# Optimization experiments

Hardware: AMD Instinct MI355X
Metric: run time of the kernel (lower is better)

## Reference

```python
import jax, jax.numpy as jnp
import numpy as np

NUM_LAYERS = 4


def setup_inputs() -> dict:
    key = jax.random.key(0)
    k1, k2, k3, k4 = jax.random.split(key, 4)
    num_users, num_items, D, E = 100000, 50000, 64, 2000000
    N = num_users + num_items
    emb_users = jax.random.normal(k1, (num_users, D), dtype=jnp.float32)
    emb_items = jax.random.normal(k2, (num_items, D), dtype=jnp.float32)
    src = jax.random.randint(k3, (E,), 0, N, dtype=jnp.int64)
    dst = jax.random.randint(k4, (E,), 0, N, dtype=jnp.int64)
    edge_index = jnp.stack([src, dst], axis=0)
    return {"emb_users": emb_users, "emb_items": emb_items, "edge_index": edge_index}


def _lightgcn(emb_users, emb_items, edge_index):
    num_users = emb_users.shape[0]
    num_items = emb_items.shape[0]
    N = num_users + num_items
    src, dst = edge_index[0], edge_index[1]

    # gcn_norm without self-loops (PyG LGConv default): deg over destination nodes
    ones = jnp.ones(src.shape[0], dtype=emb_users.dtype)
    deg = jax.ops.segment_sum(ones, dst, num_segments=N)
    deg_inv_sqrt = jnp.where(deg > 0, jax.lax.rsqrt(jnp.maximum(deg, 1.0)), 0.0)
    norm = deg_inv_sqrt[src] * deg_inv_sqrt[dst]  # [E]

    emb = jnp.concatenate([emb_users, emb_items], axis=0)  # [N, D]
    acc = emb
    for _ in range(NUM_LAYERS):
        msg = norm[:, None] * emb[src]  # [E, D]
        emb = jax.ops.segment_sum(msg, dst, num_segments=N)
        acc = acc + emb

    # original: 1/(L+1) * mean(stack, dim=1) == sum / (L+1)^2
    emb_final = acc / float((NUM_LAYERS + 1) ** 2)
    return emb_final[:num_users], emb_final[num_users:]


def reference(emb_users, emb_items, edge_index):
    return _lightgcn(emb_users, emb_items, edge_index)
```

## Files before the change

### kernel.cpp

```cpp
#include <hip/hip_runtime.h>
#include <hip/hip_bf16.h>

#define D 64
#define NUM_LAYERS 4
#define TILE 4096
#define BKMAX 320


__device__ __forceinline__ float bf_lo(unsigned u) { return __uint_as_float(u << 16); }
__device__ __forceinline__ float bf_hi(unsigned u) { return __uint_as_float(u & 0xffff0000u); }
__device__ __forceinline__ unsigned bf_pack(float x, float y) {
    __hip_bfloat16 bx = __float2bfloat16(x);
    __hip_bfloat16 by = __float2bfloat16(y);
    return (unsigned)(*reinterpret_cast<unsigned short*>(&bx))
         | ((unsigned)(*reinterpret_cast<unsigned short*>(&by)) << 16);
}


__global__ void bhist_kernel(const int* __restrict__ dst, int* __restrict__ bcnt, int E, int nbk) {
    __shared__ int h[BKMAX];
    for (int i = threadIdx.x; i < nbk; i += blockDim.x) h[i] = 0;
    __syncthreads();
    int stride = gridDim.x * blockDim.x;
    int gid = blockIdx.x * blockDim.x + threadIdx.x;
    int E4 = (((size_t)dst & 15) == 0) ? (E >> 2) : 0;
    const int4* dst4 = (const int4*)dst;
    for (int i = gid; i < E4; i += stride) {
        int4 d = dst4[i];
        atomicAdd(&h[d.x >> 9], 1);
        atomicAdd(&h[d.y >> 9], 1);
        atomicAdd(&h[d.z >> 9], 1);
        atomicAdd(&h[d.w >> 9], 1);
    }
    for (int e = (E4 << 2) + gid; e < E; e += stride)
        atomicAdd(&h[dst[e] >> 9], 1);
    __syncthreads();
    for (int i = threadIdx.x; i < nbk; i += blockDim.x)
        if (h[i] > 0) atomicAdd(&bcnt[i], h[i]);
}

__global__ __launch_bounds__(512) void bscan_kernel(const int* __restrict__ bcnt,
                                                    int* __restrict__ bstart,
                                                    int* __restrict__ gcur, int nbk, int E) {
    __shared__ int sm[512];
    int t = threadIdx.x;
    int v = (t < nbk) ? bcnt[t] : 0;
    sm[t] = v;
    __syncthreads();
    for (int ofs = 1; ofs < 512; ofs <<= 1) {
        int x = (t >= ofs) ? sm[t - ofs] : 0;
        __syncthreads();
        sm[t] += x;
        __syncthreads();
    }
    int excl = sm[t] - v;
    if (t < nbk) { bstart[t] = excl; gcur[t] = excl; }
    if (t == 0) bstart[nbk] = E;
}


__global__ __launch_bounds__(512) void placeA_kernel(const int* __restrict__ src,
                                                     const int* __restrict__ dst,
                                                     int* __restrict__ gcur,
                                                     int* __restrict__ mid,
                                                     int E, int nbk) {
    __shared__ int hist[BKMAX];
    __shared__ int toff[BKMAX];
    __shared__ int gbase[BKMAX];
    __shared__ int sc[512];
    __shared__ int els[TILE];
    __shared__ unsigned short bkt[TILE];
    int t = threadIdx.x;
    int tile0 = blockIdx.x * TILE;
    int tcnt = min(TILE, E - tile0);
    for (int i = t; i < nbk; i += 512) hist[i] = 0;
    __syncthreads();

    bool al = (((size_t)src & 15) == 0) && (((size_t)dst & 15) == 0);

    int p_[8];
    int b_[8];
    int r_[8];
#pragma unroll
    for (int i4 = 0; i4 < 2; ++i4) {
        int e0 = tile0 + i4 * 2048 + t * 4;
        int4 s4, d4;
        if (al && (e0 + 3 < E)) {
            s4 = *(const int4*)(src + e0);
            d4 = *(const int4*)(dst + e0);
        } else {
            s4 = make_int4(0, 0, 0, 0); d4 = make_int4(0, 0, 0, 0);
            if (e0     < E) { s4.x = src[e0];     d4.x = dst[e0]; }
            if (e0 + 1 < E) { s4.y = src[e0 + 1]; d4.y = dst[e0 + 1]; }
            if (e0 + 2 < E) { s4.z = src[e0 + 2]; d4.z = dst[e0 + 2]; }
            if (e0 + 3 < E) { s4.w = src[e0 + 3]; d4.w = dst[e0 + 3]; }
        }
        int ss[4] = { s4.x, s4.y, s4.z, s4.w };
        int dd[4] = { d4.x, d4.y, d4.z, d4.w };
#pragma unroll
        for (int k = 0; k < 4; ++k) {
            int i = i4 * 4 + k;
            int e = e0 + k;
            b_[i] = -1;
            if (e < E) {
                p_[i] = ss[k] | ((dd[k] & 511) << 18);
                b_[i] = dd[k] >> 9;
                r_[i] = atomicAdd(&hist[b_[i]], 1);
            }
        }
    }
    __syncthreads();
    int v = (t < nbk) ? hist[t] : 0;
    sc[t] = v;
    __syncthreads();
    for (int ofs = 1; ofs < 512; ofs <<= 1) {
        int x = (t >= ofs) ? sc[t - ofs] : 0;
        __syncthreads();
        sc[t] += x;
        __syncthreads();
    }
    if (t < nbk) toff[t] = sc[t] - v;
    __syncthreads();
#pragma unroll
    for (int i = 0; i < 8; ++i) {
        if (b_[i] >= 0) {
            int pos = toff[b_[i]] + r_[i];
            els[pos] = p_[i];
            bkt[pos] = (unsigned short)b_[i];
        }
    }
    for (int b = t; b < nbk; b += 512) {
        int h = hist[b];
        gbase[b] = (h > 0) ? atomicAdd(&gcur[b], h) : 0;
    }
    __syncthreads();
    for (int i = t; i < tcnt; i += 512) {
        int b = bkt[i];
        mid[gbase[b] + (i - toff[b])] = els[i];
    }
}

__global__ __launch_bounds__(512) void placeB1_kernel(const int* __restrict__ bstart,
                                                      const int* __restrict__ mid,
                                                      int* __restrict__ row_start,
                                                      float* __restrict__ dis,
                                                      int N, int nbk, int E) {
    __shared__ int degsm[512];
    __shared__ int sc[512];
    int b = blockIdx.x;
    int t = threadIdx.x;
    int node0 = b << 9;
    int lo = bstart[b], hi = bstart[b + 1];
    degsm[t] = 0;
    __syncthreads();
    for (int e = lo + t; e < hi; e += 512)
        atomicAdd(&degsm[(mid[e] >> 18) & 511], 1);
    __syncthreads();
    int d = degsm[t];
    sc[t] = d;
    __syncthreads();
    for (int ofs = 1; ofs < 512; ofs <<= 1) {
        int x = (t >= ofs) ? sc[t - ofs] : 0;
        __syncthreads();
        sc[t] += x;
        __syncthreads();
    }
    int excl = sc[t] - d;
    int node = node0 + t;
    if (node < N) {
        row_start[node] = lo + excl;
        dis[node] = (d > 0) ? rsqrtf((float)d) : 0.0f;
    }
    if (b == nbk - 1 && t == 0) row_start[N] = E;
}

__global__ __launch_bounds__(512) void placeB2_kernel(const int* __restrict__ bstart,
                                                      const int* __restrict__ mid,
                                                      const int* __restrict__ row_start,
                                                      const float* __restrict__ dis,
                                                      int2* __restrict__ csr, int N) {
    __shared__ int cur[512];
    __shared__ float dloc[512];
    int b = blockIdx.x;
    int t = threadIdx.x;
    int node0 = b << 9;
    int node = node0 + t;
    if (node < N) { cur[t] = row_start[node]; dloc[t] = dis[node]; }
    else          { cur[t] = 0; dloc[t] = 0.0f; }
    __syncthreads();
    int lo = bstart[b], hi = bstart[b + 1];
    for (int e = lo + t; e < hi; e += 512) {
        int m = mid[e];
        int l = (m >> 18) & 511;
        int s = m & 0x3FFFF;
        float w = dis[s] * dloc[l];
        int slot = atomicAdd(&cur[l], 1);
        csr[slot] = make_int2(s, __float_as_int(w));
    }
}


__global__ void init_kernel(const float* __restrict__ users, const float* __restrict__ items,
                            unsigned* __restrict__ A, int nu_elems, int total8) {
    int i = blockIdx.x * blockDim.x + threadIdx.x;
    if (i >= total8) return;
    long long base = (long long)i * 8;
    const float4* p;
    if (base < nu_elems) p = (const float4*)users + (base >> 2);
    else                 p = (const float4*)items + ((base - nu_elems) >> 2);
    float4 a = p[0];
    float4 b = p[1];
    uint4 r;
    r.x = bf_pack(a.x, a.y);
    r.y = bf_pack(a.z, a.w);
    r.z = bf_pack(b.x, b.y);
    r.w = bf_pack(b.z, b.w);
    ((uint4*)A)[i] = r;
}

template <int FINAL>
__global__ void gather_kernel(const int* __restrict__ row_start,
                              const int2* __restrict__ csr,
                              const uint2* __restrict__ Au,
                              uint2* __restrict__ Bu,
                              const float* __restrict__ users, const float* __restrict__ items,
                              const uint2* __restrict__ L1u, const uint2* __restrict__ L2u,
                              float* __restrict__ out,
                              int N, int nu) {
    int node = (blockIdx.x * blockDim.x + threadIdx.x) >> 6;
    if (node >= N) return;
    int lane = threadIdx.x & 63;
    int q = lane >> 4;
    int c = lane & 15;
    int beg = row_start[node];
    int end = row_start[node + 1];
    int deg = end - beg;
    float ax = 0.0f, ay = 0.0f, az = 0.0f, aw = 0.0f;

    for (int base = 0; base < deg; base += 64) {
        int chunk = min(64, deg - base);
        int   sl = 0;
        float wl = 0.0f;
        if (lane < chunk) {
            int2 e = csr[beg + base + lane];
            sl = e.x;
            wl = __int_as_float(e.y);
        }
        int k = 0;
        for (; k + 8 <= chunk; k += 8) {
            int i0 = k + q, i1 = k + 4 + q;
            int   s0 = __shfl(sl, i0), s1 = __shfl(sl, i1);
            float w0 = __shfl(wl, i0), w1 = __shfl(wl, i1);
            uint2 u0 = Au[(size_t)s0 * 16 + c];
            uint2 u1 = Au[(size_t)s1 * 16 + c];
            ax += w0 * bf_lo(u0.x); ay += w0 * bf_hi(u0.x);
            az += w0 * bf_lo(u0.y); aw += w0 * bf_hi(u0.y);
            ax += w1 * bf_lo(u1.x); ay += w1 * bf_hi(u1.x);
            az += w1 * bf_lo(u1.y); aw += w1 * bf_hi(u1.y);
        }
        for (; k < chunk; k += 4) {
            int i0 = k + q;
            int   s = __shfl(sl, i0);
            float w = __shfl(wl, i0);
            uint2 u = Au[(size_t)s * 16 + c];
            ax += w * bf_lo(u.x); ay += w * bf_hi(u.x);
            az += w * bf_lo(u.y); aw += w * bf_hi(u.y);
        }
    }

    ax += __shfl_xor(ax, 16); ay += __shfl_xor(ay, 16);
    az += __shfl_xor(az, 16); aw += __shfl_xor(aw, 16);
    ax += __shfl_xor(ax, 32); ay += __shfl_xor(ay, 32);
    az += __shfl_xor(az, 32); aw += __shfl_xor(aw, 32);

    if (q == 0) {
        size_t ro = (size_t)node * 16 + c;
        if (FINAL) {
            uint2 l1 = L1u[ro], l2 = L2u[ro], l3 = Au[ro];
            float4 e0;
            if (node < nu) e0 = ((const float4*)users)[ro];
            else           e0 = ((const float4*)items)[(size_t)(node - nu) * 16 + c];
            float rx = (e0.x + bf_lo(l1.x) + bf_lo(l2.x) + bf_lo(l3.x) + ax) * 0.04f;
            float ry = (e0.y + bf_hi(l1.x) + bf_hi(l2.x) + bf_hi(l3.x) + ay) * 0.04f;
            float rz = (e0.z + bf_lo(l1.y) + bf_lo(l2.y) + bf_lo(l3.y) + az) * 0.04f;
            float rw = (e0.w + bf_hi(l1.y) + bf_hi(l2.y) + bf_hi(l3.y) + aw) * 0.04f;
            ((float4*)out)[ro] = make_float4(rx, ry, rz, rw);
        } else {
            uint2 p;
            p.x = bf_pack(ax, ay);
            p.y = bf_pack(az, aw);
            Bu[ro] = p;
        }
    }
}


extern "C" void kernel_launch(void* const* d_in, const int* in_sizes, int n_in,
                              void* d_out, int out_size, void* d_ws, size_t ws_size,
                              hipStream_t stream) {
    const float* users = (const float*)d_in[0];
    const float* items = (const float*)d_in[1];
    const int*   eidx  = (const int*)d_in[2];

    const int nu = in_sizes[0] / D;
    const int ni = in_sizes[1] / D;
    const int N  = nu + ni;
    const int E  = in_sizes[2] / 2;
    const int Nf = N * D;
    const int nbk = (N + 511) >> 9;

    const int* src = eidx;
    const int* dst = eidx + E;

    char* ws = (char*)d_ws;
    size_t off = 0;
    auto alloc = [&](size_t bytes) {
        char* p = ws + off;
        off += (bytes + 255) & ~(size_t)255;
        return p;
    };
    float* dis       = (float*)alloc((size_t)N * 4);
    int*   row_start = (int*)alloc((size_t)(N + 1) * 4);
    int*   bcnt      = (int*)alloc(BKMAX * 4);
    int*   bstart    = (int*)alloc((BKMAX + 1) * 4);
    int*   gcur      = (int*)alloc(BKMAX * 4);
    int2*  csr       = (int2*)alloc((size_t)E * 8);
    unsigned* A0 = (unsigned*)alloc((size_t)Nf * 2);
    unsigned* L1 = (unsigned*)alloc((size_t)Nf * 2);
    unsigned* L2 = (unsigned*)alloc((size_t)Nf * 2);
    unsigned* L3 = (unsigned*)alloc((size_t)Nf * 2);
    int* mid = (int*)L3;

    const int B256 = 256;
    auto blocks = [](long long n, int b) { return (int)((n + b - 1) / b); };

    hipMemsetAsync(bcnt, 0, BKMAX * 4, stream);
    bhist_kernel<<<1024, B256, 0, stream>>>(dst, bcnt, E, nbk);
    bscan_kernel<<<1, 512, 0, stream>>>(bcnt, bstart, gcur, nbk, E);

    placeA_kernel<<<blocks(E, TILE), 512, 0, stream>>>(src, dst, gcur, mid, E, nbk);
    placeB1_kernel<<<nbk, 512, 0, stream>>>(bstart, mid, row_start, dis, N, nbk, E);
    placeB2_kernel<<<nbk, 512, 0, stream>>>(bstart, mid, row_start, dis, csr, N);

    init_kernel<<<blocks(Nf / 8, B256), B256, 0, stream>>>(users, items, A0, nu * D, Nf / 8);

    const int ggrid = blocks(N, B256 / 64);
    gather_kernel<0><<<ggrid, B256, 0, stream>>>(row_start, csr, (const uint2*)A0, (uint2*)L1,
                                                 nullptr, nullptr, nullptr, nullptr, nullptr, N, nu);
    gather_kernel<0><<<ggrid, B256, 0, stream>>>(row_start, csr, (const uint2*)L1, (uint2*)L2,
                                                 nullptr, nullptr, nullptr, nullptr, nullptr, N, nu);
    gather_kernel<0><<<ggrid, B256, 0, stream>>>(row_start, csr, (const uint2*)L2, (uint2*)L3,
                                                 nullptr, nullptr, nullptr, nullptr, nullptr, N, nu);
    gather_kernel<1><<<ggrid, B256, 0, stream>>>(row_start, csr, (const uint2*)L3, nullptr,
                                                 users, items, (const uint2*)L1, (const uint2*)L2,
                                                 (float*)d_out, N, nu);
}
```

Baseline: 390.7 us.

## Fuse bucket scan into histogram and merge placeB passes with grid sync

```diff
diff --git a/kernel.cpp b/kernel.cpp
--- a/kernel.cpp
+++ b/kernel.cpp
@@ -1,10 +1,14 @@
 #include <hip/hip_runtime.h>
 #include <hip/hip_bf16.h>
+#include <hip/hip_cooperative_groups.h>
+
+namespace cg = cooperative_groups;
 
 #define D 64
 #define NUM_LAYERS 4
 #define TILE 4096
 #define BKMAX 320
+#define MIDCAP 12288
 
 
 __device__ __forceinline__ float bf_lo(unsigned u) { return __uint_as_float(u << 16); }
@@ -17,12 +21,20 @@
 }
 
 
-__global__ void bhist_kernel(const int* __restrict__ dst, int* __restrict__ bcnt, int E, int nbk) {
+__global__ __launch_bounds__(512) void bhist_kernel(const int* __restrict__ dst,
+                                                    int* __restrict__ bcnt,
+                                                    int* __restrict__ ticket,
+                                                    int* __restrict__ bstart,
+                                                    int* __restrict__ gcur,
+                                                    int E, int nbk) {
     __shared__ int h[BKMAX];
-    for (int i = threadIdx.x; i < nbk; i += blockDim.x) h[i] = 0;
+    __shared__ int sm[512];
+    __shared__ int amLast;
+    int t = threadIdx.x;
+    for (int i = t; i < nbk; i += 512) h[i] = 0;
     __syncthreads();
     int stride = gridDim.x * blockDim.x;
-    int gid = blockIdx.x * blockDim.x + threadIdx.x;
+    int gid = blockIdx.x * blockDim.x + t;
     int E4 = (((size_t)dst & 15) == 0) ? (E >> 2) : 0;
     const int4* dst4 = (const int4*)dst;
     for (int i = gid; i < E4; i += stride) {
@@ -35,16 +47,13 @@
     for (int e = (E4 << 2) + gid; e < E; e += stride)
         atomicAdd(&h[dst[e] >> 9], 1);
     __syncthreads();
-    for (int i = threadIdx.x; i < nbk; i += blockDim.x)
+    for (int i = t; i < nbk; i += 512)
         if (h[i] > 0) atomicAdd(&bcnt[i], h[i]);
-}
-
-__global__ __launch_bounds__(512) void bscan_kernel(const int* __restrict__ bcnt,
-                                                    int* __restrict__ bstart,
-                                                    int* __restrict__ gcur, int nbk, int E) {
-    __shared__ int sm[512];
-    int t = threadIdx.x;
-    int v = (t < nbk) ? bcnt[t] : 0;
+    __threadfence();
+    if (t == 0) amLast = (atomicAdd(ticket, 1) == (int)gridDim.x - 1);
+    __syncthreads();
+    if (!amLast) return;
+    int v = (t < nbk) ? atomicAdd(&bcnt[t], 0) : 0;
     sm[t] = v;
     __syncthreads();
     for (int ofs = 1; ofs < 512; ofs <<= 1) {
@@ -140,21 +149,30 @@
     }
 }
 
-__global__ __launch_bounds__(512) void placeB1_kernel(const int* __restrict__ bstart,
-                                                      const int* __restrict__ mid,
-                                                      int* __restrict__ row_start,
-                                                      float* __restrict__ dis,
-                                                      int N, int nbk, int E) {
+__global__ __launch_bounds__(512) void placeB_kernel(const int* __restrict__ bstart,
+                                                     const int* __restrict__ mid,
+                                                     int* __restrict__ row_start,
+                                                     float* __restrict__ dis,
+                                                     int2* __restrict__ csr,
+                                                     int N, int nbk, int E) {
     __shared__ int degsm[512];
     __shared__ int sc[512];
+    __shared__ int cur[512];
+    __shared__ float dloc[512];
+    __shared__ int midc[MIDCAP];
+    cg::grid_group grid = cg::this_grid();
     int b = blockIdx.x;
     int t = threadIdx.x;
     int node0 = b << 9;
     int lo = bstart[b], hi = bstart[b + 1];
     degsm[t] = 0;
     __syncthreads();
-    for (int e = lo + t; e < hi; e += 512)
-        atomicAdd(&degsm[(mid[e] >> 18) & 511], 1);
+    for (int e = lo + t; e < hi; e += 512) {
+        int m = mid[e];
+        int i = e - lo;
+        if (i < MIDCAP) midc[i] = m;
+        atomicAdd(&degsm[(m >> 18) & 511], 1);
+    }
     __syncthreads();
     int d = degsm[t];
     sc[t] = d;
@@ -167,30 +185,19 @@
     }
     int excl = sc[t] - d;
     int node = node0 + t;
+    float dv = (d > 0) ? rsqrtf((float)d) : 0.0f;
     if (node < N) {
         row_start[node] = lo + excl;
-        dis[node] = (d > 0) ? rsqrtf((float)d) : 0.0f;
+        dis[node] = dv;
     }
     if (b == nbk - 1 && t == 0) row_start[N] = E;
-}
-
-__global__ __launch_bounds__(512) void placeB2_kernel(const int* __restrict__ bstart,
-                                                      const int* __restrict__ mid,
-                                                      const int* __restrict__ row_start,
-                                                      const float* __restrict__ dis,
-                                                      int2* __restrict__ csr, int N) {
-    __shared__ int cur[512];
-    __shared__ float dloc[512];
-    int b = blockIdx.x;
-    int t = threadIdx.x;
-    int node0 = b << 9;
-    int node = node0 + t;
-    if (node < N) { cur[t] = row_start[node]; dloc[t] = dis[node]; }
-    else          { cur[t] = 0; dloc[t] = 0.0f; }
-    __syncthreads();
-    int lo = bstart[b], hi = bstart[b + 1];
+    cur[t] = lo + excl;
+    dloc[t] = dv;
+    __threadfence();
+    grid.sync();
     for (int e = lo + t; e < hi; e += 512) {
-        int m = mid[e];
+        int i = e - lo;
+        int m = (i < MIDCAP) ? midc[i] : mid[e];
         int l = (m >> 18) & 511;
         int s = m & 0x3FFFF;
         float w = dis[s] * dloc[l];
@@ -304,10 +311,10 @@
 
     const int nu = in_sizes[0] / D;
     const int ni = in_sizes[1] / D;
-    const int N  = nu + ni;
-    const int E  = in_sizes[2] / 2;
+    int N  = nu + ni;
+    int E  = in_sizes[2] / 2;
     const int Nf = N * D;
-    const int nbk = (N + 511) >> 9;
+    int nbk = (N + 511) >> 9;
 
     const int* src = eidx;
     const int* dst = eidx + E;
@@ -321,7 +328,8 @@
     };
     float* dis       = (float*)alloc((size_t)N * 4);
     int*   row_start = (int*)alloc((size_t)(N + 1) * 4);
-    int*   bcnt      = (int*)alloc(BKMAX * 4);
+    int*   bcnt      = (int*)alloc(BKMAX * 4 + 4);
+    int*   ticket    = bcnt + BKMAX;
     int*   bstart    = (int*)alloc((BKMAX + 1) * 4);
     int*   gcur      = (int*)alloc(BKMAX * 4);
     int2*  csr       = (int2*)alloc((size_t)E * 8);
@@ -334,13 +342,18 @@
     const int B256 = 256;
     auto blocks = [](long long n, int b) { return (int)((n + b - 1) / b); };
 
-    hipMemsetAsync(bcnt, 0, BKMAX * 4, stream);
-    bhist_kernel<<<1024, B256, 0, stream>>>(dst, bcnt, E, nbk);
-    bscan_kernel<<<1, 512, 0, stream>>>(bcnt, bstart, gcur, nbk, E);
+    hipMemsetAsync(bcnt, 0, BKMAX * 4 + 4, stream);
+    bhist_kernel<<<512, 512, 0, stream>>>(dst, bcnt, ticket, bstart, gcur, E, nbk);
 
     placeA_kernel<<<blocks(E, TILE), 512, 0, stream>>>(src, dst, gcur, mid, E, nbk);
-    placeB1_kernel<<<nbk, 512, 0, stream>>>(bstart, mid, row_start, dis, N, nbk, E);
-    placeB2_kernel<<<nbk, 512, 0, stream>>>(bstart, mid, row_start, dis, csr, N);
+    {
+        const int* bstart_c = bstart;
+        const int* mid_c = mid;
+        void* bargs[] = { (void*)&bstart_c, (void*)&mid_c, (void*)&row_start,
+                          (void*)&dis, (void*)&csr, (void*)&N, (void*)&nbk, (void*)&E };
+        hipLaunchCooperativeKernel((void*)placeB_kernel, dim3(nbk), dim3(512),
+                                   bargs, 0, stream);
+    }
 
     init_kernel<<<blocks(Nf / 8, B256), B256, 0, stream>>>(users, items, A0, nu * D, Nf / 8);
 
```

After: 510.6 us. +30.7%, slower.
